# Optimization experiments

Measured on AMD Instinct MI355X. Metric: run time of the kernel, lower is better.

## Reference

```python
import jax, jax.numpy as jnp
import numpy as np

BN_EPS = 1e-5

def setup_inputs() -> dict:
    key = jax.random.key(0)
    ks = jax.random.split(key, 6)
    B, C, N = 8, 256, 4096
    da = C // 4
    return {
        "x": jax.random.normal(ks[0], (B, C, N), dtype=jnp.float32),
        "Wq": jax.random.normal(ks[1], (da, C), dtype=jnp.float32) * (C ** -0.5),
        "Wk": jax.random.normal(ks[2], (da, C), dtype=jnp.float32) * (C ** -0.5),
        "Wv": jax.random.normal(ks[3], (C, C), dtype=jnp.float32) * (C ** -0.5),
        "Wp": jax.random.normal(ks[4], (C, C), dtype=jnp.float32) * (C ** -0.5),
        "bn_gamma": jnp.ones((C,), dtype=jnp.float32),
        "bn_beta": jnp.zeros((C,), dtype=jnp.float32),
        "bn_mean": jnp.zeros((C,), dtype=jnp.float32),
        "bn_var": jnp.ones((C,), dtype=jnp.float32),
    }

def reference(x, Wq, Wk, Wv, Wp, bn_gamma, bn_beta, bn_mean, bn_var):
    # x: [B, C, N]; 1x1 Conv1d == channel matmul
    q = jnp.einsum('bcn,dc->bnd', x, Wq)          # [B, N, da]
    k = jnp.einsum('bcn,dc->bdn', x, Wk)          # [B, da, N]
    v = jnp.einsum('bcn,dc->bnd', x, Wv)          # [B, N, C]
    energy = jnp.einsum('bnd,bdm->bnm', q, k)     # [B, N, N]
    # offset-attention double normalization: softmax over dim=1 (rows), then L1 over dim=-1
    attn = jax.nn.softmax(energy, axis=1)
    attn = attn / (1e-9 + attn.sum(axis=-1, keepdims=True))
    fsa = jnp.einsum('bnm,bmc->bcn', attn, v)     # [B, C, N]
    y = x - fsa
    h = jnp.einsum('bcn,dc->bdn', y, Wp)          # 1x1 conv of LBR
    # BatchNorm1d (inference-mode with running stats)
    inv = bn_gamma / jnp.sqrt(bn_var + BN_EPS)
    h = h * inv[None, :, None] + (bn_beta - bn_mean * inv)[None, :, None]
    return jax.nn.relu(h) + x
```

## Files before the change

kernel.cpp:

```cpp
#include <hip/hip_runtime.h>
#include <math.h>

#define BD 8
#define CD 256
#define ND 4096
#define DA 64

typedef __attribute__((ext_vector_type(8))) short short8v;
typedef __attribute__((ext_vector_type(4))) float float4v;

static __device__ __forceinline__ float4v mfma16(short8v a, short8v b, float4v c) {
  return __builtin_amdgcn_mfma_f32_16x16x32_bf16(a, b, c, 0, 0, 0);
}
static __device__ __forceinline__ unsigned short f2bf(float f) {
  union { float f; unsigned int u; } v; v.f = f;
  return (unsigned short)((v.u + 0x7fffu + ((v.u >> 16) & 1u)) >> 16);
}
static __device__ __forceinline__ float bf2f(unsigned short h) {
  union { unsigned int u; float f; } v; v.u = (unsigned int)h << 16;
  return v.f;
}
static __device__ __forceinline__ int sw(int row, int c8) {
  return row * 64 + (((c8) ^ (row & 7)) << 3);
}
typedef const __attribute__((address_space(1))) unsigned int g_u32;
typedef __attribute__((address_space(3))) unsigned int l_u32;
static __device__ __forceinline__ void gld16(const void* g, void* l) {
  __builtin_amdgcn_global_load_lds((g_u32*)g, (l_u32*)l, 16, 0, 0);
}

__global__ __launch_bounds__(256) void k_prep(const float* __restrict__ x,
                                              unsigned short* __restrict__ xTh,
                                              unsigned short* __restrict__ xTl) {
  const int n0 = blockIdx.x * 64, c0 = blockIdx.y * 64, b = blockIdx.z;
  __shared__ float Xs[64][68];
  const int tid = threadIdx.x;
  const int r0 = tid >> 4, col4 = (tid & 15) * 4;
#pragma unroll
  for (int j = 0; j < 4; ++j) {
    int r = r0 + j * 16;
    *(float4*)&Xs[r][col4] =
        *(const float4*)&x[((size_t)(b * CD + c0 + r)) * ND + n0 + col4];
  }
  __syncthreads();
  const int n = tid >> 2, cg = (tid & 3) * 16;
  unsigned short h[16], l[16];
#pragma unroll
  for (int j = 0; j < 16; ++j) {
    float v = Xs[cg + j][n];
    h[j] = f2bf(v);
    l[j] = f2bf(v - bf2f(h[j]));
  }
  size_t o = ((size_t)b * ND + n0 + n) * CD + c0 + cg;
#pragma unroll
  for (int j = 0; j < 4; ++j) {
    *(ushort4*)&xTh[o + j * 4] = *(ushort4*)&h[j * 4];
    *(ushort4*)&xTl[o + j * 4] = *(ushort4*)&l[j * 4];
  }
}

__global__ void k_prepW(const float* __restrict__ Wq, const float* __restrict__ Wk,
                        const float* __restrict__ Wv, const float* __restrict__ Wp,
                        unsigned short* Wch, unsigned short* Wcl,
                        unsigned short* Wph, unsigned short* Wpl) {
  int i = blockIdx.x * 256 + threadIdx.x;
  int row = i >> 6, c4 = (i & 63) * 4;
  const float* src; unsigned short *dh, *dl; int r, drow;
  if (row < 64)       { src = Wq; r = row;       dh = Wch; dl = Wcl; drow = row; }
  else if (row < 128) { src = Wk; r = row - 64;  dh = Wch; dl = Wcl; drow = row; }
  else if (row < 384) { src = Wv; r = row - 128; dh = Wch; dl = Wcl; drow = row; }
  else                { src = Wp; r = row - 384; dh = Wph; dl = Wpl; drow = row - 384; }
  float4 f = *(const float4*)&src[(size_t)r * 256 + c4];
  ushort4 hh, ll;
  hh.x = f2bf(f.x); hh.y = f2bf(f.y); hh.z = f2bf(f.z); hh.w = f2bf(f.w);
  ll.x = f2bf(f.x - bf2f(hh.x)); ll.y = f2bf(f.y - bf2f(hh.y));
  ll.z = f2bf(f.z - bf2f(hh.z)); ll.w = f2bf(f.w - bf2f(hh.w));
  *(ushort4*)&dh[(size_t)drow * 256 + c4] = hh;
  *(ushort4*)&dl[(size_t)drow * 256 + c4] = ll;
}

__global__ __launch_bounds__(512) void k_proj(
    const unsigned short* __restrict__ xTh, const unsigned short* __restrict__ xTl,
    const unsigned short* __restrict__ Wch, const unsigned short* __restrict__ Wcl,
    unsigned short* __restrict__ qh, unsigned short* __restrict__ kh,
    unsigned short* __restrict__ kl, unsigned short* __restrict__ vT) {
  const int n0 = blockIdx.x * 128, b = blockIdx.y;
  const int tid = threadIdx.x, w = tid >> 6, lane = tid & 63, lq = lane & 15,
            quad = lane >> 4;
  __shared__ __align__(16) unsigned short xs[2][2][128][40];
  float4v O[24];
#pragma unroll
  for (int t = 0; t < 24; ++t) O[t] = (float4v){0.f, 0.f, 0.f, 0.f};

  const int srow = tid >> 2, sc4 = tid & 3;
  uint4 rh, rl;
  auto load_slice = [&](int ks) {
    size_t a = ((size_t)b * ND + n0 + srow) * CD + ks * 32 + sc4 * 8;
    rh = *(const uint4*)(xTh + a);
    rl = *(const uint4*)(xTl + a);
  };
  auto write_slice = [&](int buf) {
    *(uint4*)&xs[buf][0][srow][sc4 * 8] = rh;
    *(uint4*)&xs[buf][1][srow][sc4 * 8] = rl;
  };
  load_slice(0); write_slice(0);
#pragma unroll 1
  for (int ks = 0; ks < 8; ++ks) {
    __syncthreads();
    if (ks < 7) load_slice(ks + 1);
    short8v bxh = *(const short8v*)&xs[ks & 1][0][w * 16 + lq][quad * 8];
    short8v bxl = *(const short8v*)&xs[ks & 1][1][w * 16 + lq][quad * 8];
#pragma unroll
    for (int t = 0; t < 24; ++t) {
      size_t a = (size_t)(t * 16 + lq) * CD + ks * 32 + quad * 8;
      short8v awh = *(const short8v*)(Wch + a);
      short8v awl = *(const short8v*)(Wcl + a);
      O[t] = mfma16(awh, bxh, O[t]);
      O[t] = mfma16(awl, bxh, O[t]);
      O[t] = mfma16(awh, bxl, O[t]);
    }
    if (ks < 7) write_slice((ks + 1) & 1);
  }
  const int n = n0 + w * 16 + lq;
#pragma unroll
  for (int t = 0; t < 24; ++t) {
    if (t < 4) {
      ushort4 hh;
      hh.x = f2bf(O[t][0]); hh.y = f2bf(O[t][1]);
      hh.z = f2bf(O[t][2]); hh.w = f2bf(O[t][3]);
      *(ushort4*)&qh[((size_t)b * ND + n) * DA + t * 16 + quad * 4] = hh;
    } else if (t < 8) {
      ushort4 hh, ll;
      hh.x = f2bf(O[t][0]); hh.y = f2bf(O[t][1]);
      hh.z = f2bf(O[t][2]); hh.w = f2bf(O[t][3]);
      ll.x = f2bf(O[t][0] - bf2f(hh.x)); ll.y = f2bf(O[t][1] - bf2f(hh.y));
      ll.z = f2bf(O[t][2] - bf2f(hh.z)); ll.w = f2bf(O[t][3] - bf2f(hh.w));
      size_t o = ((size_t)b * ND + n) * DA + (t - 4) * 16 + quad * 4;
      *(ushort4*)&kh[o] = hh;
      *(ushort4*)&kl[o] = ll;
    } else {
#pragma unroll
      for (int r = 0; r < 4; ++r) {
        int c = (t - 8) * 16 + quad * 4 + r;
        vT[((size_t)b * CD + c) * ND + n] = f2bf(O[t][r]);
      }
    }
  }
}

__global__ __launch_bounds__(512, 4) void k_colsum(
    const unsigned short* __restrict__ qh, const unsigned short* __restrict__ khp,
    const unsigned short* __restrict__ klp, float* __restrict__ Dp) {
  const int bid = blockIdx.x, b = bid & 7, half = (bid >> 3) & 1,
            m0 = (bid >> 4) * 128;
  const int nbase = half * 2048;
  const int tid = threadIdx.x, w = tid >> 6, lane = tid & 63, lq = lane & 15,
            quad = lane >> 4;
  const int mq = w & 3, nh = w >> 2;
  __shared__ __align__(16) unsigned short qbuf[3][4096];
  __shared__ float Cb[128];
  short8v bkh[2][2], bkl[2][2];
#pragma unroll
  for (int sub = 0; sub < 2; ++sub)
#pragma unroll
    for (int k = 0; k < 2; ++k) {
      size_t a = ((size_t)b * ND + m0 + mq * 32 + sub * 16 + lq) * DA + k * 32 + quad * 8;
      bkh[sub][k] = *(const short8v*)(khp + a);
      bkl[sub][k] = *(const short8v*)(klp + a);
    }
  const int srow = w * 8 + (lane >> 3), sck = lane & 7;
  auto stageQ = [&](int it, int qn) {
    const unsigned short* src = qh + ((size_t)b * ND + nbase + it * 64 + srow) * DA +
                                ((sck ^ (srow & 7)) << 3);
    gld16(src, &qbuf[qn][0] + (size_t)w * 512);
  };
  stageQ(0, 0);
  stageQ(1, 1);
  asm volatile("s_waitcnt vmcnt(1)\n\ts_barrier" ::: "memory");
  float cs0 = 0.f, cs1 = 0.f;
  int rc = 0, sc = 2;
#pragma unroll 1
  for (int i = 0; i < 32; ++i) {
    if (i < 30) { stageQ(i + 2, sc); sc = (sc + 1 == 3) ? 0 : sc + 1; }
#pragma unroll
    for (int s = 0; s < 2; ++s) {
      short8v ah[2];
#pragma unroll
      for (int k = 0; k < 2; ++k)
        ah[k] = *(const short8v*)&qbuf[rc][sw(nh * 32 + s * 16 + lq, k * 4 + quad)];
#pragma unroll
      for (int sub = 0; sub < 2; ++sub) {
        float4v acc = {0.f, 0.f, 0.f, 0.f};
#pragma unroll
        for (int k = 0; k < 2; ++k) {
          acc = mfma16(ah[k], bkh[sub][k], acc);
          acc = mfma16(ah[k], bkl[sub][k], acc);
        }
        float e0 = __expf(acc[0]) + __expf(acc[1]) + __expf(acc[2]) + __expf(acc[3]);
        if (sub == 0) cs0 += e0; else cs1 += e0;
      }
    }
    rc = (rc + 1 == 3) ? 0 : rc + 1;
    if (i < 30)
      asm volatile("s_waitcnt vmcnt(1) lgkmcnt(0)\n\ts_barrier" ::: "memory");
    else
      asm volatile("s_waitcnt vmcnt(0) lgkmcnt(0)\n\ts_barrier" ::: "memory");
  }
  cs0 += __shfl_down(cs0, 16); cs0 += __shfl_down(cs0, 32);
  cs1 += __shfl_down(cs1, 16); cs1 += __shfl_down(cs1, 32);
  if (nh == 0 && lane < 16) {
    Cb[mq * 32 + lane] = cs0;
    Cb[mq * 32 + 16 + lane] = cs1;
  }
  __syncthreads();
  if (nh == 1 && lane < 16) {
    float t0 = Cb[mq * 32 + lane] + cs0;
    float t1 = Cb[mq * 32 + 16 + lane] + cs1;
    size_t o = (size_t)half * (BD * ND) + (size_t)b * ND + m0 + mq * 32 + lane;
    Dp[o] = t0;
    Dp[o + 16] = t1;
  }
}

__global__ void k_rcp(const float* __restrict__ Dp, float* __restrict__ Drec) {
  int i = blockIdx.x * 256 + threadIdx.x;
  float4 a = *(const float4*)&Dp[(size_t)i * 4];
  float4 c = *(const float4*)&Dp[(size_t)(BD * ND) + (size_t)i * 4];
  float4 r;
  r.x = 1.f / (a.x + c.x); r.y = 1.f / (a.y + c.y);
  r.z = 1.f / (a.z + c.z); r.w = 1.f / (a.w + c.w);
  *(float4*)&Drec[(size_t)i * 4] = r;
}

__global__ __launch_bounds__(1024, 4) void k_attn(
    const unsigned short* __restrict__ qh, const unsigned short* __restrict__ khp,
    const unsigned short* __restrict__ klp, const unsigned short* __restrict__ vT,
    const float* __restrict__ Drec, unsigned short* xhy,
    const unsigned short* __restrict__ xTl) {
  const int bid = blockIdx.x, b = bid & 7, n0 = (bid >> 3) * 128;
  const int tid = threadIdx.x, w = tid >> 6, lane = tid & 63, lq = lane & 15,
            quad = lane >> 4;
  const int nq = w & 3, cq = w >> 2;
  __shared__ __align__(16) unsigned short vbuf[3][16384];
  __shared__ __align__(16) unsigned short Pb[2][8192];
  __shared__ float Sb4[4][128];

  short8v aq[2][2];
#pragma unroll
  for (int s = 0; s < 2; ++s)
#pragma unroll
    for (int k = 0; k < 2; ++k)
      aq[s][k] = *(const short8v*)(qh + ((size_t)b * ND + n0 + nq * 32 + s * 16 + lq) * DA +
                                   k * 32 + quad * 8);
  float4v O[2][4];
#pragma unroll
  for (int s = 0; s < 2; ++s)
#pragma unroll
    for (int t = 0; t < 4; ++t) O[s][t] = (float4v){0.f, 0.f, 0.f, 0.f};
  float rs[2] = {0.f, 0.f};

  auto stageV = [&](int mt, int vn) {
    unsigned short* base = &vbuf[vn][0];
#pragma unroll
    for (int j = 0; j < 2; ++j) {
      int cidx = tid + j * 1024;
      int row = cidx >> 3, ckpos = cidx & 7;
      const unsigned short* src =
          vT + ((size_t)b * CD + row) * ND + mt * 64 + ((ckpos ^ (row & 7)) << 3);
      gld16(src, base + (size_t)(w * 64 + j * 1024) * 8);
    }
  };
  short8v kc[4], kn[4];
  auto kload = [&](short8v* dst, int mt) {
#pragma unroll
    for (int k = 0; k < 2; ++k) {
      size_t a = ((size_t)b * ND + mt * 64 + cq * 16 + lq) * DA + k * 32 + quad * 8;
      dst[k * 2 + 0] = *(const short8v*)(khp + a);
      dst[k * 2 + 1] = *(const short8v*)(klp + a);
    }
  };
  auto doPV = [&](const unsigned short* Pc, const unsigned short* vc) {
    short8v ap[2][2];
#pragma unroll
    for (int s = 0; s < 2; ++s)
#pragma unroll
      for (int k = 0; k < 2; ++k)
        ap[s][k] = *(const short8v*)&Pc[sw(nq * 32 + s * 16 + lq, k * 4 + quad)];
#pragma unroll
    for (int t = 0; t < 4; ++t) {
      const int trow = (cq * 4 + t) * 16 + lq;
#pragma unroll
      for (int k = 0; k < 2; ++k) {
        short8v bv = *(const short8v*)&vc[sw(trow, k * 4 + quad)];
#pragma unroll
        for (int s = 0; s < 2; ++s) O[s][t] = mfma16(bv, ap[s][k], O[s][t]);
      }
    }
  };

  float4 drc4, drn4;
  stageV(0, 0);
  kload(kc, 0);
  drc4 = *(const float4*)&Drec[(size_t)b * ND + cq * 16 + quad * 4];

  int vs = 1, vp = 0;
#pragma unroll 1
  for (int i = 0; i < 64; ++i) {
    if (i > 0) {
      doPV(&Pb[(i - 1) & 1][0], &vbuf[vp][0]);
      vp = (vp + 1 == 3) ? 0 : vp + 1;
    }
    if (i < 63) {
      kload(kn, i + 1);
      drn4 = *(const float4*)&Drec[(size_t)b * ND + (i + 1) * 64 + cq * 16 + quad * 4];
      stageV(i + 1, vs);
      vs = (vs + 1 == 3) ? 0 : vs + 1;
    }
    unsigned short* Pcur = &Pb[i & 1][0];
#pragma unroll
    for (int s = 0; s < 2; ++s) {
      float4v acc = {0.f, 0.f, 0.f, 0.f};
#pragma unroll
      for (int k = 0; k < 2; ++k) {
        acc = mfma16(kc[k * 2 + 0], aq[s][k], acc);
        acc = mfma16(kc[k * 2 + 1], aq[s][k], acc);
      }
      float p0 = __expf(acc[0]) * drc4.x;
      float p1 = __expf(acc[1]) * drc4.y;
      float p2 = __expf(acc[2]) * drc4.z;
      float p3 = __expf(acc[3]) * drc4.w;
      rs[s] += (p0 + p1) + (p2 + p3);
      unsigned int w0 =
          (__float_as_uint(p0) >> 16) | (__float_as_uint(p1) & 0xffff0000u);
      unsigned int w1 =
          (__float_as_uint(p2) >> 16) | (__float_as_uint(p3) & 0xffff0000u);
      const int nl = nq * 32 + s * 16 + lq;
      const int c8 = cq * 2 + (quad >> 1);
      uint2 wv; wv.x = w0; wv.y = w1;
      *(uint2*)&Pcur[nl * 64 + ((c8 ^ (nl & 7)) << 3) + ((quad & 1) << 2)] = wv;
    }
    if (i < 63) {
#pragma unroll
      for (int t = 0; t < 4; ++t) kc[t] = kn[t];
      drc4 = drn4;
    }
    if (i < 63)
      asm volatile("s_waitcnt vmcnt(2) lgkmcnt(0)\n\ts_barrier" ::: "memory");
    else
      asm volatile("s_waitcnt vmcnt(0) lgkmcnt(0)\n\ts_barrier" ::: "memory");
  }
  doPV(&Pb[1][0], &vbuf[vp][0]);

  rs[0] += __shfl_xor(rs[0], 16); rs[0] += __shfl_xor(rs[0], 32);
  rs[1] += __shfl_xor(rs[1], 16); rs[1] += __shfl_xor(rs[1], 32);
  if (lane < 16) {
    Sb4[cq][nq * 32 + lane] = rs[0];
    Sb4[cq][nq * 32 + 16 + lane] = rs[1];
  }
  __syncthreads();
  float rsc[2];
#pragma unroll
  for (int s = 0; s < 2; ++s) {
    const int nloc = nq * 32 + s * 16 + lq;
    rsc[s] = 1.0f / (1e-9f + Sb4[0][nloc] + Sb4[1][nloc] + Sb4[2][nloc] + Sb4[3][nloc]);
  }
#pragma unroll
  for (int t = 0; t < 4; ++t) {
    const int cb = (cq * 4 + t) * 16 + quad * 4;
#pragma unroll
    for (int s = 0; s < 2; ++s) {
      const int n = n0 + nq * 32 + s * 16 + lq;
      const size_t off = ((size_t)b * ND + n) * CD + cb;
      ushort4 h4 = *(const ushort4*)&xhy[off];
      ushort4 l4 = *(const ushort4*)&xTl[off];
      ushort4 o4;
      o4.x = f2bf(bf2f(h4.x) + bf2f(l4.x) - O[s][t][0] * rsc[s]);
      o4.y = f2bf(bf2f(h4.y) + bf2f(l4.y) - O[s][t][1] * rsc[s]);
      o4.z = f2bf(bf2f(h4.z) + bf2f(l4.z) - O[s][t][2] * rsc[s]);
      o4.w = f2bf(bf2f(h4.w) + bf2f(l4.w) - O[s][t][3] * rsc[s]);
      *(ushort4*)&xhy[off] = o4;
    }
  }
}

__global__ __launch_bounds__(256) void k_final(const unsigned short* __restrict__ y,
                                               const unsigned short* __restrict__ Wpb,
                                               const float* __restrict__ x,
                                               const float* __restrict__ gamma,
                                               const float* __restrict__ beta,
                                               const float* __restrict__ mean,
                                               const float* __restrict__ var,
                                               float* __restrict__ out) {
  const int bid = blockIdx.x;
  const int b = bid & 7;
  const int rem = bid >> 3;
  const int n0 = (rem & 63) * 64;
  const int d0 = (rem >> 6) * 64;
  const int tid = threadIdx.x;
  const int wave = tid >> 6, lane = tid & 63, lq = lane & 15, quad = lane >> 4;
  const int dw = d0 + wave * 16;
  float4v O[4];
#pragma unroll
  for (int s = 0; s < 4; ++s) O[s] = (float4v){0.f, 0.f, 0.f, 0.f};
#pragma unroll
  for (int chh = 0; chh < 8; ++chh) {
    const size_t ab = (size_t)(dw + lq) * CD + chh * 32 + quad * 8;
    short8v a0 = *(const short8v*)(Wpb + ab);
#pragma unroll
    for (int s = 0; s < 4; ++s) {
      const size_t bb = ((size_t)b * ND + n0 + s * 16 + lq) * CD + chh * 32 + quad * 8;
      short8v bv = *(const short8v*)(y + bb);
      O[s] = mfma16(a0, bv, O[s]);
    }
  }
#pragma unroll
  for (int r = 0; r < 4; ++r) {
    const int d = dw + quad * 4 + r;
    const float inv  = gamma[d] / sqrtf(var[d] + 1e-5f);
    const float bias = beta[d] - mean[d] * inv;
#pragma unroll
    for (int s = 0; s < 4; ++s) {
      const int n = n0 + s * 16 + lq;
      const size_t oi = ((size_t)b * CD + d) * ND + n;
      out[oi] = fmaxf(O[s][r] * inv + bias, 0.f) + x[oi];
    }
  }
}

extern "C" void kernel_launch(void* const* d_in, const int* in_sizes, int n_in,
                              void* d_out, int out_size, void* d_ws, size_t ws_size,
                              hipStream_t stream) {
  const float* x     = (const float*)d_in[0];
  const float* Wq    = (const float*)d_in[1];
  const float* Wk    = (const float*)d_in[2];
  const float* Wv    = (const float*)d_in[3];
  const float* Wp    = (const float*)d_in[4];
  const float* gamma = (const float*)d_in[5];
  const float* beta  = (const float*)d_in[6];
  const float* mean  = (const float*)d_in[7];
  const float* var   = (const float*)d_in[8];
  float* out = (float*)d_out;

  char* wsp = (char*)d_ws;
  unsigned short* qhp = (unsigned short*)wsp; wsp += (size_t)BD * ND * DA * 2;
  unsigned short* khp = (unsigned short*)wsp; wsp += (size_t)BD * ND * DA * 2;
  unsigned short* klp = (unsigned short*)wsp; wsp += (size_t)BD * ND * DA * 2;
  unsigned short* vT  = (unsigned short*)wsp; wsp += (size_t)BD * CD * ND * 2;
  unsigned short* xTh = (unsigned short*)wsp; wsp += (size_t)BD * ND * CD * 2;
  unsigned short* xTl = (unsigned short*)wsp; wsp += (size_t)BD * ND * CD * 2;
  unsigned short* Wch = (unsigned short*)wsp; wsp += (size_t)384 * 256 * 2;
  unsigned short* Wcl = (unsigned short*)wsp; wsp += (size_t)384 * 256 * 2;
  unsigned short* Wph = (unsigned short*)wsp; wsp += (size_t)256 * 256 * 2;
  unsigned short* Wpl = (unsigned short*)wsp; wsp += (size_t)256 * 256 * 2;
  float* Drec = (float*)wsp; wsp += (size_t)BD * ND * 4;
  float* Dp   = (float*)wsp; wsp += (size_t)2 * BD * ND * 4;
  unsigned short* y = xTh;

  dim3 blk(256), blk5(512), blkA(1024);
  k_prep<<<dim3(ND / 64, CD / 64, BD), blk, 0, stream>>>(x, xTh, xTl);
  k_prepW<<<dim3(160), blk, 0, stream>>>(Wq, Wk, Wv, Wp, Wch, Wcl, Wph, Wpl);
  k_proj<<<dim3(ND / 128, BD), blk5, 0, stream>>>(xTh, xTl, Wch, Wcl, qhp, khp,
                                                  klp, vT);
  k_colsum<<<dim3(512), blk5, 0, stream>>>(qhp, khp, klp, Dp);
  k_rcp<<<dim3(32), blk, 0, stream>>>(Dp, Drec);
  k_attn<<<dim3(256), blkA, 0, stream>>>(qhp, khp, klp, vT, Drec, y, xTl);
  k_final<<<dim3(2048), blk, 0, stream>>>(y, Wph, x, gamma, beta, mean, var, out);
}
```

Baseline: 492.3 us.

## Halve attention block to 512 threads with larger per-wave output tiles

The attention kernel now runs 8 waves instead of 16 per block. Each wave owns a 64-row by 64-channel output tile instead of 32 by 64, so the P and V fragments loaded from LDS are reused across more MFMAs. This also means fewer waves meet at each barrier. In exchange each wave holds more accumulator registers, issues more global loads for V staging, and the block has less parallelism to hide latency. The vmcnt wait count is adjusted to match the extra in-flight loads.

```diff
diff --git a/kernel.cpp b/kernel.cpp
--- a/kernel.cpp
+++ b/kernel.cpp
@@ -232,7 +232,7 @@
   *(float4*)&Drec[(size_t)i * 4] = r;
 }
 
-__global__ __launch_bounds__(1024, 4) void k_attn(
+__global__ __launch_bounds__(512, 2) void k_attn(
     const unsigned short* __restrict__ qh, const unsigned short* __restrict__ khp,
     const unsigned short* __restrict__ klp, const unsigned short* __restrict__ vT,
     const float* __restrict__ Drec, unsigned short* xhy,
@@ -240,60 +240,58 @@
   const int bid = blockIdx.x, b = bid & 7, n0 = (bid >> 3) * 128;
   const int tid = threadIdx.x, w = tid >> 6, lane = tid & 63, lq = lane & 15,
             quad = lane >> 4;
-  const int nq = w & 3, cq = w >> 2;
+  const int nh = w & 1, mt = w >> 1;
   __shared__ __align__(16) unsigned short vbuf[3][16384];
   __shared__ __align__(16) unsigned short Pb[2][8192];
   __shared__ float Sb4[4][128];
 
-  short8v aq[2][2];
-#pragma unroll
-  for (int s = 0; s < 2; ++s)
+  short8v aq[4][2];
+#pragma unroll
+  for (int s = 0; s < 4; ++s)
 #pragma unroll
     for (int k = 0; k < 2; ++k)
-      aq[s][k] = *(const short8v*)(qh + ((size_t)b * ND + n0 + nq * 32 + s * 16 + lq) * DA +
+      aq[s][k] = *(const short8v*)(qh + ((size_t)b * ND + n0 + nh * 64 + s * 16 + lq) * DA +
                                    k * 32 + quad * 8);
-  float4v O[2][4];
-#pragma unroll
-  for (int s = 0; s < 2; ++s)
-#pragma unroll
-    for (int t = 0; t < 4; ++t) O[s][t] = (float4v){0.f, 0.f, 0.f, 0.f};
-  float rs[2] = {0.f, 0.f};
-
-  auto stageV = [&](int mt, int vn) {
+  float4v O[4][4];
+#pragma unroll
+  for (int ct = 0; ct < 4; ++ct)
+#pragma unroll
+    for (int s = 0; s < 4; ++s) O[ct][s] = (float4v){0.f, 0.f, 0.f, 0.f};
+  float rs[4] = {0.f, 0.f, 0.f, 0.f};
+
+  auto stageV = [&](int mtile, int vn) {
     unsigned short* base = &vbuf[vn][0];
 #pragma unroll
-    for (int j = 0; j < 2; ++j) {
-      int cidx = tid + j * 1024;
+    for (int j = 0; j < 4; ++j) {
+      int cidx = tid + j * 512;
       int row = cidx >> 3, ckpos = cidx & 7;
       const unsigned short* src =
-          vT + ((size_t)b * CD + row) * ND + mt * 64 + ((ckpos ^ (row & 7)) << 3);
-      gld16(src, base + (size_t)(w * 64 + j * 1024) * 8);
+          vT + ((size_t)b * CD + row) * ND + mtile * 64 + ((ckpos ^ (row & 7)) << 3);
+      gld16(src, base + (size_t)(w * 64 + j * 512) * 8);
     }
   };
   short8v kc[4], kn[4];
-  auto kload = [&](short8v* dst, int mt) {
+  auto kload = [&](short8v* dst, int mtile) {
 #pragma unroll
     for (int k = 0; k < 2; ++k) {
-      size_t a = ((size_t)b * ND + mt * 64 + cq * 16 + lq) * DA + k * 32 + quad * 8;
+      size_t a = ((size_t)b * ND + mtile * 64 + mt * 16 + lq) * DA + k * 32 + quad * 8;
       dst[k * 2 + 0] = *(const short8v*)(khp + a);
       dst[k * 2 + 1] = *(const short8v*)(klp + a);
     }
   };
   auto doPV = [&](const unsigned short* Pc, const unsigned short* vc) {
-    short8v ap[2][2];
-#pragma unroll
-    for (int s = 0; s < 2; ++s)
-#pragma unroll
-      for (int k = 0; k < 2; ++k)
-        ap[s][k] = *(const short8v*)&Pc[sw(nq * 32 + s * 16 + lq, k * 4 + quad)];
-#pragma unroll
-    for (int t = 0; t < 4; ++t) {
-      const int trow = (cq * 4 + t) * 16 + lq;
-#pragma unroll
-      for (int k = 0; k < 2; ++k) {
-        short8v bv = *(const short8v*)&vc[sw(trow, k * 4 + quad)];
-#pragma unroll
-        for (int s = 0; s < 2; ++s) O[s][t] = mfma16(bv, ap[s][k], O[s][t]);
+#pragma unroll
+    for (int ks = 0; ks < 2; ++ks) {
+      short8v ap[4];
+#pragma unroll
+      for (int s = 0; s < 4; ++s)
+        ap[s] = *(const short8v*)&Pc[sw(nh * 64 + s * 16 + lq, ks * 4 + quad)];
+#pragma unroll
+      for (int ct = 0; ct < 4; ++ct) {
+        const int trow = (mt * 4 + ct) * 16 + lq;
+        short8v bv = *(const short8v*)&vc[sw(trow, ks * 4 + quad)];
+#pragma unroll
+        for (int s = 0; s < 4; ++s) O[ct][s] = mfma16(bv, ap[s], O[ct][s]);
       }
     }
   };
@@ -301,7 +299,7 @@
   float4 drc4, drn4;
   stageV(0, 0);
   kload(kc, 0);
-  drc4 = *(const float4*)&Drec[(size_t)b * ND + cq * 16 + quad * 4];
+  drc4 = *(const float4*)&Drec[(size_t)b * ND + mt * 16 + quad * 4];
 
   int vs = 1, vp = 0;
 #pragma unroll 1
@@ -312,13 +310,13 @@
     }
     if (i < 63) {
       kload(kn, i + 1);
-      drn4 = *(const float4*)&Drec[(size_t)b * ND + (i + 1) * 64 + cq * 16 + quad * 4];
+      drn4 = *(const float4*)&Drec[(size_t)b * ND + (i + 1) * 64 + mt * 16 + quad * 4];
       stageV(i + 1, vs);
       vs = (vs + 1 == 3) ? 0 : vs + 1;
     }
     unsigned short* Pcur = &Pb[i & 1][0];
 #pragma unroll
-    for (int s = 0; s < 2; ++s) {
+    for (int s = 0; s < 4; ++s) {
       float4v acc = {0.f, 0.f, 0.f, 0.f};
 #pragma unroll
       for (int k = 0; k < 2; ++k) {
@@ -334,8 +332,8 @@
           (__float_as_uint(p0) >> 16) | (__float_as_uint(p1) & 0xffff0000u);
       unsigned int w1 =
           (__float_as_uint(p2) >> 16) | (__float_as_uint(p3) & 0xffff0000u);
-      const int nl = nq * 32 + s * 16 + lq;
-      const int c8 = cq * 2 + (quad >> 1);
+      const int nl = nh * 64 + s * 16 + lq;
+      const int c8 = mt * 2 + (quad >> 1);
       uint2 wv; wv.x = w0; wv.y = w1;
       *(uint2*)&Pcur[nl * 64 + ((c8 ^ (nl & 7)) << 3) + ((quad & 1) << 2)] = wv;
     }
@@ -345,39 +343,42 @@
       drc4 = drn4;
     }
     if (i < 63)
-      asm volatile("s_waitcnt vmcnt(2) lgkmcnt(0)\n\ts_barrier" ::: "memory");
+      asm volatile("s_waitcnt vmcnt(4) lgkmcnt(0)\n\ts_barrier" ::: "memory");
     else
       asm volatile("s_waitcnt vmcnt(0) lgkmcnt(0)\n\ts_barrier" ::: "memory");
   }
   doPV(&Pb[1][0], &vbuf[vp][0]);
 
-  rs[0] += __shfl_xor(rs[0], 16); rs[0] += __shfl_xor(rs[0], 32);
-  rs[1] += __shfl_xor(rs[1], 16); rs[1] += __shfl_xor(rs[1], 32);
+#pragma unroll
+  for (int s = 0; s < 4; ++s) {
+    rs[s] += __shfl_xor(rs[s], 16);
+    rs[s] += __shfl_xor(rs[s], 32);
+  }
   if (lane < 16) {
-    Sb4[cq][nq * 32 + lane] = rs[0];
-    Sb4[cq][nq * 32 + 16 + lane] = rs[1];
+#pragma unroll
+    for (int s = 0; s < 4; ++s) Sb4[mt][nh * 64 + s * 16 + lane] = rs[s];
   }
   __syncthreads();
-  float rsc[2];
-#pragma unroll
-  for (int s = 0; s < 2; ++s) {
-    const int nloc = nq * 32 + s * 16 + lq;
+  float rsc[4];
+#pragma unroll
+  for (int s = 0; s < 4; ++s) {
+    const int nloc = nh * 64 + s * 16 + lq;
     rsc[s] = 1.0f / (1e-9f + Sb4[0][nloc] + Sb4[1][nloc] + Sb4[2][nloc] + Sb4[3][nloc]);
   }
 #pragma unroll
-  for (int t = 0; t < 4; ++t) {
-    const int cb = (cq * 4 + t) * 16 + quad * 4;
-#pragma unroll
-    for (int s = 0; s < 2; ++s) {
-      const int n = n0 + nq * 32 + s * 16 + lq;
+  for (int ct = 0; ct < 4; ++ct) {
+    const int cb = (mt * 4 + ct) * 16 + quad * 4;
+#pragma unroll
+    for (int s = 0; s < 4; ++s) {
+      const int n = n0 + nh * 64 + s * 16 + lq;
       const size_t off = ((size_t)b * ND + n) * CD + cb;
       ushort4 h4 = *(const ushort4*)&xhy[off];
       ushort4 l4 = *(const ushort4*)&xTl[off];
       ushort4 o4;
-      o4.x = f2bf(bf2f(h4.x) + bf2f(l4.x) - O[s][t][0] * rsc[s]);
-      o4.y = f2bf(bf2f(h4.y) + bf2f(l4.y) - O[s][t][1] * rsc[s]);
-      o4.z = f2bf(bf2f(h4.z) + bf2f(l4.z) - O[s][t][2] * rsc[s]);
-      o4.w = f2bf(bf2f(h4.w) + bf2f(l4.w) - O[s][t][3] * rsc[s]);
+      o4.x = f2bf(bf2f(h4.x) + bf2f(l4.x) - O[ct][s][0] * rsc[s]);
+      o4.y = f2bf(bf2f(h4.y) + bf2f(l4.y) - O[ct][s][1] * rsc[s]);
+      o4.z = f2bf(bf2f(h4.z) + bf2f(l4.z) - O[ct][s][2] * rsc[s]);
+      o4.w = f2bf(bf2f(h4.w) + bf2f(l4.w) - O[ct][s][3] * rsc[s]);
       *(ushort4*)&xhy[off] = o4;
     }
   }
@@ -456,13 +457,13 @@
   float* Dp   = (float*)wsp; wsp += (size_t)2 * BD * ND * 4;
   unsigned short* y = xTh;
 
-  dim3 blk(256), blk5(512), blkA(1024);
+  dim3 blk(256), blk5(512);
   k_prep<<<dim3(ND / 64, CD / 64, BD), blk, 0, stream>>>(x, xTh, xTl);
   k_prepW<<<dim3(160), blk, 0, stream>>>(Wq, Wk, Wv, Wp, Wch, Wcl, Wph, Wpl);
   k_proj<<<dim3(ND / 128, BD), blk5, 0, stream>>>(xTh, xTl, Wch, Wcl, qhp, khp,
                                                   klp, vT);
   k_colsum<<<dim3(512), blk5, 0, stream>>>(qhp, khp, klp, Dp);
   k_rcp<<<dim3(32), blk, 0, stream>>>(Dp, Drec);
-  k_attn<<<dim3(256), blkA, 0, stream>>>(qhp, khp, klp, vT, Drec, y, xTl);
+  k_attn<<<dim3(256), blk5, 0, stream>>>(qhp, khp, klp, vT, Drec, y, xTl);
   k_final<<<dim3(2048), blk, 0, stream>>>(y, Wph, x, gamma, beta, mean, var, out);
 }
```

After: 443.9 us. 1.11x faster.
